# Optimization experiments

Hardware: AMD Instinct MI355X
Metric: run time of the kernel (lower is better)

Reference implementation:

```python
import jax, jax.numpy as jnp
import numpy as np

H, W, D, HEADS = 32, 32, 16, 8
EPS = 1e-5

def _ln(x, g, b):
    m = jnp.mean(x, -1, keepdims=True)
    v = jnp.mean((x - m) ** 2, -1, keepdims=True)
    return (x - m) / jnp.sqrt(v + EPS) * g + b

def _attn(x, w_qkv, w_proj, b_proj):
    # x: (Bb, N, C); torch Linear: y = x @ W.T + b
    Bb, N, C = x.shape
    hd = C // HEADS
    qkv = jnp.einsum('bnc,dc->bnd', x, w_qkv).reshape(Bb, N, 3, HEADS, hd)
    q, k, v = qkv[:, :, 0], qkv[:, :, 1], qkv[:, :, 2]  # (Bb,N,h,hd)
    att = jnp.einsum('bnhd,bmhd->bhnm', q, k) * (hd ** -0.5)
    att = jax.nn.softmax(att, axis=-1)
    o = jnp.einsum('bhnm,bmhd->bnhd', att, v).reshape(Bb, N, C)
    return jnp.einsum('bnc,dc->bnd', o, w_proj) + b_proj

def setup_inputs() -> dict:
    key = jax.random.key(0)
    ks = jax.random.split(key, 8)
    C, HID = 96, 384
    s = 0.02
    return {
        'x': jax.random.normal(ks[0], (1, C, D, H, W), jnp.float32),
        'norm1_g': jnp.ones((C,), jnp.float32),
        'norm1_b': jnp.zeros((C,), jnp.float32),
        'qkv_hw_w': jax.random.normal(ks[1], (3 * C, C), jnp.float32) * s,
        'proj_hw_w': jax.random.normal(ks[2], (C, C), jnp.float32) * s,
        'proj_hw_b': jnp.zeros((C,), jnp.float32),
        'qkv_t_w': jax.random.normal(ks[3], (3 * C, C), jnp.float32) * s,
        'proj_t_w': jax.random.normal(ks[4], (C, C), jnp.float32) * s,
        'proj_t_b': jnp.zeros((C,), jnp.float32),
        'norm2_g': jnp.ones((C,), jnp.float32),
        'norm2_b': jnp.zeros((C,), jnp.float32),
        'fc1_w': jax.random.normal(ks[5], (HID, C), jnp.float32) * s,
        'fc1_b': jnp.zeros((HID,), jnp.float32),
        'fc2_w': jax.random.normal(ks[6], (C, HID), jnp.float32) * s,
        'fc2_b': jnp.zeros((C,), jnp.float32),
    }

def reference(x, norm1_g, norm1_b, qkv_hw_w, proj_hw_w, proj_hw_b,
              qkv_t_w, proj_t_w, proj_t_b, norm2_g, norm2_b,
              fc1_w, fc1_b, fc2_w, fc2_b):
    B, C = x.shape[0], x.shape[1]
    HWn = H * W
    xf = x.reshape(B, C, -1).transpose(0, 2, 1)  # (B, L, C), L = D*H*W (D-major)
    shortcut = xf
    n1 = _ln(xf, norm1_g, norm1_b).reshape(B, D, HWn, C)
    # attention over H*W tokens (batched over B*D)
    a_hw = _attn(n1.reshape(B * D, HWn, C), qkv_hw_w, proj_hw_w, proj_hw_b)
    a_hw = a_hw.reshape(B, -1, C)  # D-major token order
    # attention over D tokens (batched over B*H*W)
    a_t = _attn(n1.transpose(0, 2, 1, 3).reshape(B * HWn, D, C), qkv_t_w, proj_t_w, proj_t_b)
    a_t = a_t.reshape(B, HWn * D, C)  # HW-major order (faithful to original view)
    out_res = shortcut + a_hw + a_t
    h1 = jax.nn.gelu(jnp.einsum('blc,hc->blh', _ln(out_res, norm2_g, norm2_b), fc1_w) + fc1_b,
                     approximate=False)
    mlp_out = jnp.einsum('blh,ch->blc', h1, fc2_w) + fc2_b
    out_ffn = out_res + mlp_out
    out = out_ffn.reshape(B, H, W, D, C).transpose(0, 4, 3, 1, 2)  # (B,C,D,H,W)
    return out
```

## Files before the change

### kernel.cpp

```cpp
#include <hip/hip_runtime.h>
#include <math.h>

#define L_TOK 16384
#define C_DIM 96
#define N_HEADS 8
#define HD 12
#define D_DIM 16
#define HW_N 1024
#define HID_DIM 384
#define SCALE 0.2886751345948129f
#define LOG2E 1.4426950408889634f

typedef _Float16 h4 __attribute__((ext_vector_type(4)));
typedef __fp16 fp16x2 __attribute__((ext_vector_type(2)));
typedef float v4f __attribute__((ext_vector_type(4)));

static __device__ __forceinline__ float fast_exp2(float x) {
#if __has_builtin(__builtin_amdgcn_exp2f)
    return __builtin_amdgcn_exp2f(x);
#else
    float r;
    asm("v_exp_f32 %0, %1" : "=v"(r) : "v"(x));
    return r;
#endif
}

static __device__ __forceinline__ h4 pack4(float a, float b, float c, float d) {
    fp16x2 lo = __builtin_amdgcn_cvt_pkrtz(a, b);
    fp16x2 hi = __builtin_amdgcn_cvt_pkrtz(c, d);
    union { fp16x2 p[2]; h4 v; } u;
    u.p[0] = lo; u.p[1] = hi;
    return u.v;
}

__global__ __launch_bounds__(256) void prep_kernel(
    const float* __restrict__ x, const float* __restrict__ g1,
    const float* __restrict__ b1, _Float16* __restrict__ n1h,
    const float* __restrict__ qkv_hw_w, const float* __restrict__ qkv_t_w,
    const float* __restrict__ proj_hw_w, const float* __restrict__ proj_t_w,
    const float* __restrict__ proj_hw_b, const float* __restrict__ proj_t_b,
    const float* __restrict__ fc1_w, const float* __restrict__ fc2_w,
    _Float16* __restrict__ wq, _Float16* __restrict__ wp,
    _Float16* __restrict__ wf1, _Float16* __restrict__ wf2,
    float* __restrict__ bp) {
    if (blockIdx.x < 64) {
        int l = blockIdx.x * 256 + threadIdx.x;
        float v[C_DIM];
        float s = 0.f;
#pragma unroll
        for (int c = 0; c < C_DIM; c++) {
            v[c] = x[(size_t)c * L_TOK + l];
            s += v[c];
        }
        float mean = s * (1.f / C_DIM);
        float var = 0.f;
#pragma unroll
        for (int c = 0; c < C_DIM; c++) {
            float dd = v[c] - mean;
            var += dd * dd;
        }
        float r = rsqrtf(var * (1.f / C_DIM) + 1e-5f);
        _Float16* op = n1h + (size_t)l * C_DIM;
#pragma unroll
        for (int c = 0; c < C_DIM; c += 4) {
            h4 o;
            o[0] = (_Float16)((v[c + 0] - mean) * r * g1[c + 0] + b1[c + 0]);
            o[1] = (_Float16)((v[c + 1] - mean) * r * g1[c + 1] + b1[c + 1]);
            o[2] = (_Float16)((v[c + 2] - mean) * r * g1[c + 2] + b1[c + 2]);
            o[3] = (_Float16)((v[c + 3] - mean) * r * g1[c + 3] + b1[c + 3]);
            *(h4*)(op + c) = o;
        }
        return;
    }
    int idx = (blockIdx.x - 64) * 256 + threadIdx.x;
    if (idx < 55296) {
        int n = idx / 96;
        float v = (n < 288) ? qkv_hw_w[idx] : qkv_t_w[idx - 27648];
        bool isq = (n < 96) || (n >= 288 && n < 384);
        wq[idx] = (_Float16)(isq ? v * (SCALE * LOG2E) : v);
    } else if (idx < 55296 + 18432) {
        int i = idx - 55296;
        int n = i / 192, k = i % 192;
        float v = (k < 96) ? proj_hw_w[n * 96 + k] : proj_t_w[n * 96 + k - 96];
        wp[i] = (_Float16)v;
    } else if (idx < 73728 + 36864) {
        int i = idx - 73728;
        wf1[i] = (_Float16)fc1_w[i];
    } else if (idx < 110592 + 36864) {
        int i = idx - 110592;
        wf2[i] = (_Float16)fc2_w[i];
    } else if (idx < 147456 + 96) {
        int i = idx - 147456;
        bp[i] = proj_hw_b[i] + proj_t_b[i];
    }
}

#define GBM 64
#define GBN 48
#define GBK 96
#define LSTRIDE 104

__global__ __launch_bounds__(256) void gemm_qkv(
    const _Float16* __restrict__ A, const _Float16* __restrict__ W,
    _Float16* __restrict__ Qp, _Float16* __restrict__ Kp,
    _Float16* __restrict__ VTp, _Float16* __restrict__ Tp) {
    __shared__ _Float16 As[GBM][LSTRIDE];
    __shared__ _Float16 Ws[GBN][LSTRIDE];
    const int t = threadIdx.x;
    const int m0 = blockIdx.x * GBM;
    const int n0 = blockIdx.y * GBN;
    const int lane = t & 63, w = t >> 6, g = lane >> 4, r = lane & 15;

    v4f acc[3];
#pragma unroll
    for (int nt = 0; nt < 3; nt++) {
        acc[nt][0] = 0.f; acc[nt][1] = 0.f; acc[nt][2] = 0.f; acc[nt][3] = 0.f;
    }
#pragma unroll
    for (int i = 0; i < 3; i++) {
        int idx = t + i * 256;
        int row = idx / 12, c = idx % 12;
        *(float4*)&As[row][c * 8] =
            *(const float4*)&A[(size_t)(m0 + row) * 96 + c * 8];
    }
#pragma unroll
    for (int i = 0; i < 3; i++) {
        int idx = t + i * 256;
        if (idx < 576) {
            int row = idx / 12, c = idx % 12;
            *(float4*)&Ws[row][c * 8] =
                *(const float4*)&W[(size_t)(n0 + row) * 96 + c * 8];
        }
    }
    __syncthreads();
#pragma unroll
    for (int ks = 0; ks < 6; ks++) {
        h4 af = *(const h4*)&As[w * 16 + r][ks * 16 + 4 * g];
#pragma unroll
        for (int nt = 0; nt < 3; nt++) {
            h4 wf = *(const h4*)&Ws[nt * 16 + r][ks * 16 + 4 * g];
            acc[nt] = __builtin_amdgcn_mfma_f32_16x16x16f16(wf, af, acc[nt], 0, 0, 0);
        }
    }

    const int m = m0 + w * 16 + r;
    const int d = m >> 10, hw = m & 1023;
    const int by = blockIdx.y;
#pragma unroll
    for (int nt = 0; nt < 3; nt++) {
        const int nb = n0 + nt * 16 + 4 * g;
        h4 ov;
        ov[0] = (_Float16)acc[nt][0]; ov[1] = (_Float16)acc[nt][1];
        ov[2] = (_Float16)acc[nt][2]; ov[3] = (_Float16)acc[nt][3];
        if (by < 2) {
            int n = nb;
            int h = (unsigned)n / 12u, dd = n - h * 12;
            *(h4*)&Qp[((size_t)(d * 8 + h) * 1024 + hw) * 12 + dd] = ov;
        } else if (by < 4) {
            int n = nb - 96;
            int h = (unsigned)n / 12u, dd = n - h * 12;
            *(h4*)&Kp[((size_t)(d * 8 + h) * 1024 + hw) * 12 + dd] = ov;
        } else if (by < 6) {
            int n = nb - 192;
            int h = (unsigned)n / 12u, dd = n - h * 12;
#pragma unroll
            for (int j = 0; j < 4; j++) {
                VTp[((size_t)(d * 8 + h) * 12 + dd + j) * 1024 + hw] = ov[j];
            }
        } else {
            *(h4*)&Tp[(size_t)(hw * 16 + d) * 288 + (nb - 288)] = ov;
        }
    }
}

#define WSTRIDE 104

#define STAGE(buf, src, stride)                                              \
    {                                                                        \
        _Pragma("unroll")                                                    \
        for (int i_ = 0; i_ < 5; i_++) {                                     \
            int idx_ = t + i_ * 256;                                         \
            if (idx_ < 1152) {                                               \
                int row_ = idx_ / 12, c_ = idx_ % 12;                        \
                *(float4*)&Wb[buf][row_ * WSTRIDE + c_ * 8] =                \
                    *(const float4*)&(src)[(size_t)row_ * (stride) + c_ * 8];\
            }                                                                \
        }                                                                    \
    }

#define PROJ_CHUNK(buf, kc)                                                  \
    {                                                                        \
        _Pragma("unroll")                                                    \
        for (int ks = 0; ks < 6; ks++) {                                     \
            _Pragma("unroll")                                                \
            for (int nt = 0; nt < 6; nt++) {                                 \
                h4 wf = *(const h4*)&Wb[buf][(nt * 16 + r) * WSTRIDE +       \
                                             ks * 16 + 4 * g];               \
                acc[nt] = __builtin_amdgcn_mfma_f32_16x16x16f16(             \
                    wf, afp[kc][ks], acc[nt], 0, 0, 0);                      \
            }                                                                \
        }                                                                    \
    }

#define FC1_CHUNK(buf, nc)                                                   \
    {                                                                        \
        v4f f[6];                                                            \
        _Pragma("unroll")                                                    \
        for (int nt = 0; nt < 6; nt++) {                                     \
            f[nt][0] = 0.f; f[nt][1] = 0.f; f[nt][2] = 0.f; f[nt][3] = 0.f;  \
        }                                                                    \
        _Pragma("unroll")                                                    \
        for (int ks = 0; ks < 6; ks++) {                                     \
            _Pragma("unroll")                                                \
            for (int nt = 0; nt < 6; nt++) {                                 \
                h4 wf = *(const h4*)&Wb[buf][(nt * 16 + r) * WSTRIDE +       \
                                             ks * 16 + 4 * g];               \
                f[nt] = __builtin_amdgcn_mfma_f32_16x16x16f16(               \
                    wf, n2f[ks], f[nt], 0, 0, 0);                            \
            }                                                                \
        }                                                                    \
        _Pragma("unroll")                                                    \
        for (int nt = 0; nt < 6; nt++) {                                     \
            const int nb = (nc) * 96 + nt * 16 + 4 * g;                      \
            float4 bv = *(const float4*)&f1b[nb];                            \
            float u0 = f[nt][0] + bv.x, u1 = f[nt][1] + bv.y;                \
            float u2 = f[nt][2] + bv.z, u3 = f[nt][3] + bv.w;                \
            hf[nc][nt] =                                                     \
                pack4(0.5f * u0 * (1.f + erff(u0 * 0.7071067811865476f)),    \
                      0.5f * u1 * (1.f + erff(u1 * 0.7071067811865476f)),    \
                      0.5f * u2 * (1.f + erff(u2 * 0.7071067811865476f)),    \
                      0.5f * u3 * (1.f + erff(u3 * 0.7071067811865476f)));   \
        }                                                                    \
    }

#define FC2_CHUNK(buf, kc)                                                   \
    {                                                                        \
        _Pragma("unroll")                                                    \
        for (int ks = 0; ks < 6; ks++) {                                     \
            _Pragma("unroll")                                                \
            for (int nt = 0; nt < 6; nt++) {                                 \
                h4 wf = *(const h4*)&Wb[buf][(nt * 16 + r) * WSTRIDE +       \
                                             ks * 16 + 4 * g];               \
                o6[nt] = __builtin_amdgcn_mfma_f32_16x16x16f16(              \
                    wf, hf[kc][ks], o6[nt], 0, 0, 0);                        \
            }                                                                \
        }                                                                    \
    }

__global__ __launch_bounds__(256) void fused_mlp(
    const _Float16* __restrict__ A, const _Float16* __restrict__ wp,
    const float* __restrict__ bp, const float* __restrict__ x,
    const float* __restrict__ g2, const float* __restrict__ b2,
    const _Float16* __restrict__ wf1, const float* __restrict__ f1b,
    const _Float16* __restrict__ wf2, const float* __restrict__ f2b,
    float* __restrict__ out) {
    __shared__ _Float16 Wb[2][96 * WSTRIDE];
    __shared__ float sh[96 * 68];

    const int t = threadIdx.x;
    const int bx = blockIdx.x;
    const int bxs = (bx & 7) * 32 + (bx >> 3);
    const int m0 = bxs * 64;
    const int lane = t & 63, w = t >> 6, g = lane >> 4, r = lane & 15;
    const int ml = w * 16 + r;
    const int m = m0 + ml;

    h4 afp[2][6];
#pragma unroll
    for (int kc = 0; kc < 2; kc++)
#pragma unroll
        for (int ks = 0; ks < 6; ks++)
            afp[kc][ks] =
                *(const h4*)&A[(size_t)m * 192 + kc * 96 + ks * 16 + 4 * g];
    float xr[24];
#pragma unroll
    for (int nt = 0; nt < 6; nt++) {
#pragma unroll
        for (int j = 0; j < 4; j++)
            xr[nt * 4 + j] = x[(size_t)(nt * 16 + 4 * g + j) * L_TOK + m];
    }

    STAGE(0, wp, 192);
    __syncthreads();
    STAGE(1, wp + 96, 192);
    v4f acc[6];
#pragma unroll
    for (int nt = 0; nt < 6; nt++) {
        acc[nt][0] = 0.f; acc[nt][1] = 0.f; acc[nt][2] = 0.f; acc[nt][3] = 0.f;
    }
    PROJ_CHUNK(0, 0);
    __syncthreads();
    STAGE(0, wf1, 96);
    PROJ_CHUNK(1, 1);
    float v[24];
    float sum = 0.f;
#pragma unroll
    for (int nt = 0; nt < 6; nt++) {
        const int nb = nt * 16 + 4 * g;
        float4 bv = *(const float4*)&bp[nb];
        float a0 = acc[nt][0] + bv.x + xr[nt * 4 + 0];
        float a1 = acc[nt][1] + bv.y + xr[nt * 4 + 1];
        float a2 = acc[nt][2] + bv.z + xr[nt * 4 + 2];
        float a3 = acc[nt][3] + bv.w + xr[nt * 4 + 3];
        v[nt * 4 + 0] = a0; v[nt * 4 + 1] = a1;
        v[nt * 4 + 2] = a2; v[nt * 4 + 3] = a3;
        sum += (a0 + a1) + (a2 + a3);
    }
    sum += __shfl_xor(sum, 16, 64);
    sum += __shfl_xor(sum, 32, 64);
    float mean = sum * (1.f / 96.f);
    float ss = 0.f;
#pragma unroll
    for (int i = 0; i < 24; i++) {
        float dd = v[i] - mean;
        ss += dd * dd;
    }
    ss += __shfl_xor(ss, 16, 64);
    ss += __shfl_xor(ss, 32, 64);
    float rstd = rsqrtf(ss * (1.f / 96.f) + 1e-5f);
    h4 n2f[6];
#pragma unroll
    for (int nt = 0; nt < 6; nt++) {
        const int nb = nt * 16 + 4 * g;
        float4 gg = *(const float4*)&g2[nb];
        float4 bb = *(const float4*)&b2[nb];
        n2f[nt] = pack4((v[nt * 4 + 0] - mean) * rstd * gg.x + bb.x,
                        (v[nt * 4 + 1] - mean) * rstd * gg.y + bb.y,
                        (v[nt * 4 + 2] - mean) * rstd * gg.z + bb.z,
                        (v[nt * 4 + 3] - mean) * rstd * gg.w + bb.w);
    }
    __syncthreads();
    h4 hf[4][6];
    STAGE(1, wf1 + 96 * 96, 96);
    FC1_CHUNK(0, 0);
    __syncthreads();
    STAGE(0, wf1 + 2 * 96 * 96, 96);
    FC1_CHUNK(1, 1);
    __syncthreads();
    STAGE(1, wf1 + 3 * 96 * 96, 96);
    FC1_CHUNK(0, 2);
    __syncthreads();
    STAGE(0, wf2, 384);
    FC1_CHUNK(1, 3);
    __syncthreads();
    v4f o6[6];
#pragma unroll
    for (int nt = 0; nt < 6; nt++) {
        o6[nt][0] = 0.f; o6[nt][1] = 0.f; o6[nt][2] = 0.f; o6[nt][3] = 0.f;
    }
    STAGE(1, wf2 + 96, 384);
    FC2_CHUNK(0, 0);
    __syncthreads();
    STAGE(0, wf2 + 192, 384);
    FC2_CHUNK(1, 1);
    __syncthreads();
    STAGE(1, wf2 + 288, 384);
    FC2_CHUNK(0, 2);
    __syncthreads();
    FC2_CHUNK(1, 3);

#pragma unroll
    for (int nt = 0; nt < 6; nt++) {
        const int nb = nt * 16 + 4 * g;
        float4 bv = *(const float4*)&f2b[nb];
        sh[(nb + 0) * 68 + ml] = o6[nt][0] + bv.x + v[nt * 4 + 0];
        sh[(nb + 1) * 68 + ml] = o6[nt][1] + bv.y + v[nt * 4 + 1];
        sh[(nb + 2) * 68 + ml] = o6[nt][2] + bv.z + v[nt * 4 + 2];
        sh[(nb + 3) * 68 + ml] = o6[nt][3] + bv.w + v[nt * 4 + 3];
    }
    __syncthreads();
    const int hh = m0 >> 9, ww0 = (m0 >> 4) & 31;
#pragma unroll
    for (int i = 0; i < 6; i++) {
        int task = t + i * 256;
        int n = task >> 4, dd = task & 15;
        float4 ov;
        ov.x = sh[n * 68 + dd];
        ov.y = sh[n * 68 + dd + 16];
        ov.z = sh[n * 68 + dd + 32];
        ov.w = sh[n * 68 + dd + 48];
        *(float4*)&out[(size_t)n * L_TOK + dd * 1024 + hh * 32 + ww0] = ov;
    }
}

__global__ __launch_bounds__(256) void attn_hw_kernel(
    const _Float16* __restrict__ Qp, const _Float16* __restrict__ Kp,
    const _Float16* __restrict__ VTp, _Float16* __restrict__ o_cat) {
    __shared__ _Float16 K_lds[1024 * 12];
    __shared__ _Float16 VT_lds[13 * 1032];
    const int t = threadIdx.x;
    const int qb = blockIdx.x, h = blockIdx.y, d = blockIdx.z;
    const size_t tokbase = (size_t)d * HW_N;
    const int hoff = h * HD;
    const size_t slice = (size_t)(d * 8 + h);

    {
        const float4* Kg = (const float4*)(Kp + slice * 12288);
        float4* K4 = (float4*)K_lds;
#pragma unroll
        for (int i = 0; i < 6; i++) K4[t + i * 256] = Kg[t + i * 256];
        const float4* Vg = (const float4*)(VTp + slice * 12288);
#pragma unroll
        for (int i = 0; i < 6; i++) {
            int off = t + i * 256;
            int row = off >> 7, col = (off & 127) * 8;
            *(float4*)&VT_lds[row * 1032 + col] = Vg[off];
        }
        unsigned* zp = (unsigned*)&VT_lds[12 * 1032];
        zp[t] = 0x3C003C00u; zp[t + 256] = 0x3C003C00u;
        if (t < 4) zp[t + 512] = 0x3C003C00u;
    }

    const int lane = t & 63, w = t >> 6, g = lane >> 4, r = lane & 15;
    const int q0w = qb * 128 + w * 32;

    h4 zf; zf[0] = zf[1] = zf[2] = zf[3] = (_Float16)0.f;
    h4 qf[2];
    {
        const _Float16* Qbase = Qp + (slice * 1024 + q0w + r) * 12 + 4 * g;
#pragma unroll
        for (int qt = 0; qt < 2; qt++) {
            qf[qt] = (g < 3) ? *(const h4*)(Qbase + qt * 16 * 12) : zf;
        }
    }

    v4f acc[2];
#pragma unroll
    for (int qt = 0; qt < 2; qt++) {
        acc[qt][0] = acc[qt][1] = acc[qt][2] = acc[qt][3] = 0.f;
    }

    const int koff = r * 12 + 4 * g;
    const int rowc = (r < 12) ? r : 12;
    const int voff = rowc * 1032 + 4 * g;

    __syncthreads();

    v4f zero; zero[0] = zero[1] = zero[2] = zero[3] = 0.f;
#pragma unroll 4
    for (int kt = 0; kt < HW_N / 16; kt++) {
        h4 kf = (g < 3) ? *(const h4*)&K_lds[kt * 192 + koff] : zf;
        h4 vf = *(const h4*)&VT_lds[voff + kt * 16];
#pragma unroll
        for (int qt = 0; qt < 2; qt++) {
            v4f s = __builtin_amdgcn_mfma_f32_16x16x16f16(kf, qf[qt], zero, 0, 0, 0);
            h4 pf = pack4(fast_exp2(s[0]), fast_exp2(s[1]),
                          fast_exp2(s[2]), fast_exp2(s[3]));
            acc[qt] = __builtin_amdgcn_mfma_f32_16x16x16f16(vf, pf, acc[qt], 0, 0, 0);
        }
    }

#pragma unroll
    for (int qt = 0; qt < 2; qt++) {
        float denom = __shfl(acc[qt][0], 48 + r, 64);
        float rs = 1.f / denom;
        if (g < 3) {
            _Float16* op =
                o_cat + (tokbase + q0w + qt * 16 + r) * 192 + hoff + 4 * g;
            h4 o;
            o[0] = (_Float16)(acc[qt][0] * rs);
            o[1] = (_Float16)(acc[qt][1] * rs);
            o[2] = (_Float16)(acc[qt][2] * rs);
            o[3] = (_Float16)(acc[qt][3] * rs);
            *(h4*)op = o;
        }
    }
}

__global__ __launch_bounds__(256) void attn_t_kernel(
    const _Float16* __restrict__ Tp, _Float16* __restrict__ o_cat) {
    int gid = blockIdx.x * 256 + threadIdx.x;
    int hw = gid >> 7;
    int h = (gid >> 4) & 7;
    int q = gid & 15;
    const int hoff = h * HD;
    const _Float16* base = Tp + (size_t)(hw * 16) * 288;

    float qr[HD];
    {
        const _Float16* p = base + q * 288 + hoff;
        h4 a = *(const h4*)p, b = *(const h4*)(p + 4), c = *(const h4*)(p + 8);
#pragma unroll
        for (int e = 0; e < 4; e++) {
            qr[e] = (float)a[e]; qr[4 + e] = (float)b[e]; qr[8 + e] = (float)c[e];
        }
    }
    float s[D_DIM];
    float mx = -1e30f;
#pragma unroll
    for (int j = 0; j < D_DIM; j++) {
        const _Float16* kp = base + j * 288 + 96 + hoff;
        h4 a = *(const h4*)kp, b = *(const h4*)(kp + 4), c = *(const h4*)(kp + 8);
        float dot = 0.f;
#pragma unroll
        for (int e = 0; e < 4; e++) {
            dot += qr[e] * (float)a[e] + qr[4 + e] * (float)b[e] +
                   qr[8 + e] * (float)c[e];
        }
        s[j] = dot;
        mx = fmaxf(mx, dot);
    }
    float sum = 0.f;
#pragma unroll
    for (int j = 0; j < D_DIM; j++) {
        s[j] = fast_exp2(s[j] - mx);
        sum += s[j];
    }
    float rs = 1.f / sum;
    float o[HD];
#pragma unroll
    for (int e = 0; e < HD; e++) o[e] = 0.f;
#pragma unroll
    for (int j = 0; j < D_DIM; j++) {
        const _Float16* vp = base + j * 288 + 192 + hoff;
        h4 a = *(const h4*)vp, b = *(const h4*)(vp + 4), c = *(const h4*)(vp + 8);
        float p = s[j];
#pragma unroll
        for (int e = 0; e < 4; e++) {
            o[e] += p * (float)a[e];
            o[4 + e] += p * (float)b[e];
            o[8 + e] += p * (float)c[e];
        }
    }
    _Float16* op = o_cat + ((size_t)hw * D_DIM + q) * 192 + 96 + hoff;
#pragma unroll
    for (int e = 0; e < HD; e += 4) {
        h4 a;
        a[0] = (_Float16)(o[e] * rs); a[1] = (_Float16)(o[e + 1] * rs);
        a[2] = (_Float16)(o[e + 2] * rs); a[3] = (_Float16)(o[e + 3] * rs);
        *(h4*)(op + e) = a;
    }
}

extern "C" void kernel_launch(void* const* d_in, const int* in_sizes, int n_in,
                              void* d_out, int out_size, void* d_ws,
                              size_t ws_size, hipStream_t stream) {
    const float* x         = (const float*)d_in[0];
    const float* norm1_g   = (const float*)d_in[1];
    const float* norm1_b   = (const float*)d_in[2];
    const float* qkv_hw_w  = (const float*)d_in[3];
    const float* proj_hw_w = (const float*)d_in[4];
    const float* proj_hw_b = (const float*)d_in[5];
    const float* qkv_t_w   = (const float*)d_in[6];
    const float* proj_t_w  = (const float*)d_in[7];
    const float* proj_t_b  = (const float*)d_in[8];
    const float* norm2_g   = (const float*)d_in[9];
    const float* norm2_b   = (const float*)d_in[10];
    const float* fc1_w     = (const float*)d_in[11];
    const float* fc1_b     = (const float*)d_in[12];
    const float* fc2_w     = (const float*)d_in[13];
    const float* fc2_b     = (const float*)d_in[14];
    float* out = (float*)d_out;

    char* ws = (char*)d_ws;
    _Float16* n1h    = (_Float16*)ws;
    _Float16* o_cat  = n1h + (size_t)L_TOK * C_DIM;
    float*    out_res= (float*)(o_cat + (size_t)L_TOK * 192);
    _Float16* packs  = (_Float16*)(out_res + (size_t)L_TOK * C_DIM);
    _Float16* Qp     = packs;
    _Float16* Kp     = Qp + 1572864;
    _Float16* VTp    = Kp + 1572864;
    _Float16* Tp     = VTp + 1572864;
    _Float16* wq     = Tp + (size_t)L_TOK * 288;
    _Float16* wp     = wq + 55296;
    _Float16* wf1    = wp + 18432;
    _Float16* wf2    = wf1 + 36864;
    float*    bp     = (float*)(wf2 + 36864);

    prep_kernel<<<641, 256, 0, stream>>>(x, norm1_g, norm1_b, n1h,
                                         qkv_hw_w, qkv_t_w, proj_hw_w,
                                         proj_t_w, proj_hw_b, proj_t_b,
                                         fc1_w, fc2_w, wq, wp, wf1, wf2, bp);
    gemm_qkv<<<dim3(L_TOK / GBM, 576 / GBN), 256, 0, stream>>>(
        n1h, wq, Qp, Kp, VTp, Tp);
    attn_hw_kernel<<<dim3(8, N_HEADS, D_DIM), 256, 0, stream>>>(
        Qp, Kp, VTp, o_cat);
    attn_t_kernel<<<(HW_N * N_HEADS * D_DIM) / 256, 256, 0, stream>>>(Tp, o_cat);
    fused_mlp<<<L_TOK / 64, 256, 0, stream>>>(
        o_cat, wp, bp, x, norm2_g, norm2_b, wf1, fc1_b, wf2, fc2_b, out);
}
```

Before: 92.83 us.

## Halve fused MLP tile to 32 tokens and alias output staging onto weight LDS

```diff
diff --git a/kernel.cpp b/kernel.cpp
--- a/kernel.cpp
+++ b/kernel.cpp
@@ -174,28 +174,29 @@
 }
 
 #define WSTRIDE 104
+#define SH_STRIDE 42
 
 #define STAGE(buf, src, stride)                                              \
     {                                                                        \
+        _Float16* Wb_ = (buf) ? Wb1 : Wb0;                                   \
         _Pragma("unroll")                                                    \
-        for (int i_ = 0; i_ < 5; i_++) {                                     \
-            int idx_ = t + i_ * 256;                                         \
-            if (idx_ < 1152) {                                               \
-                int row_ = idx_ / 12, c_ = idx_ % 12;                        \
-                *(float4*)&Wb[buf][row_ * WSTRIDE + c_ * 8] =                \
-                    *(const float4*)&(src)[(size_t)row_ * (stride) + c_ * 8];\
-            }                                                                \
+        for (int i_ = 0; i_ < 9; i_++) {                                     \
+            int idx_ = t + i_ * 128;                                         \
+            int row_ = idx_ / 12, c_ = idx_ % 12;                            \
+            *(float4*)&Wb_[row_ * WSTRIDE + c_ * 8] =                        \
+                *(const float4*)&(src)[(size_t)row_ * (stride) + c_ * 8];    \
         }                                                                    \
     }
 
 #define PROJ_CHUNK(buf, kc)                                                  \
     {                                                                        \
+        const _Float16* Wb_ = (buf) ? Wb1 : Wb0;                             \
         _Pragma("unroll")                                                    \
         for (int ks = 0; ks < 6; ks++) {                                     \
             _Pragma("unroll")                                                \
             for (int nt = 0; nt < 6; nt++) {                                 \
-                h4 wf = *(const h4*)&Wb[buf][(nt * 16 + r) * WSTRIDE +       \
-                                             ks * 16 + 4 * g];               \
+                h4 wf = *(const h4*)&Wb_[(nt * 16 + r) * WSTRIDE +           \
+                                         ks * 16 + 4 * g];                   \
                 acc[nt] = __builtin_amdgcn_mfma_f32_16x16x16f16(             \
                     wf, afp[kc][ks], acc[nt], 0, 0, 0);                      \
             }                                                                \
@@ -204,6 +205,7 @@
 
 #define FC1_CHUNK(buf, nc)                                                   \
     {                                                                        \
+        const _Float16* Wb_ = (buf) ? Wb1 : Wb0;                             \
         v4f f[6];                                                            \
         _Pragma("unroll")                                                    \
         for (int nt = 0; nt < 6; nt++) {                                     \
@@ -213,8 +215,8 @@
         for (int ks = 0; ks < 6; ks++) {                                     \
             _Pragma("unroll")                                                \
             for (int nt = 0; nt < 6; nt++) {                                 \
-                h4 wf = *(const h4*)&Wb[buf][(nt * 16 + r) * WSTRIDE +       \
-                                             ks * 16 + 4 * g];               \
+                h4 wf = *(const h4*)&Wb_[(nt * 16 + r) * WSTRIDE +           \
+                                         ks * 16 + 4 * g];                   \
                 f[nt] = __builtin_amdgcn_mfma_f32_16x16x16f16(               \
                     wf, n2f[ks], f[nt], 0, 0, 0);                            \
             }                                                                \
@@ -235,32 +237,35 @@
 
 #define FC2_CHUNK(buf, kc)                                                   \
     {                                                                        \
+        const _Float16* Wb_ = (buf) ? Wb1 : Wb0;                             \
         _Pragma("unroll")                                                    \
         for (int ks = 0; ks < 6; ks++) {                                     \
             _Pragma("unroll")                                                \
             for (int nt = 0; nt < 6; nt++) {                                 \
-                h4 wf = *(const h4*)&Wb[buf][(nt * 16 + r) * WSTRIDE +       \
-                                             ks * 16 + 4 * g];               \
+                h4 wf = *(const h4*)&Wb_[(nt * 16 + r) * WSTRIDE +           \
+                                         ks * 16 + 4 * g];                   \
                 o6[nt] = __builtin_amdgcn_mfma_f32_16x16x16f16(              \
                     wf, hf[kc][ks], o6[nt], 0, 0, 0);                        \
             }                                                                \
         }                                                                    \
     }
 
-__global__ __launch_bounds__(256) void fused_mlp(
+__global__ __launch_bounds__(128, 2) void fused_mlp(
     const _Float16* __restrict__ A, const _Float16* __restrict__ wp,
     const float* __restrict__ bp, const float* __restrict__ x,
     const float* __restrict__ g2, const float* __restrict__ b2,
     const _Float16* __restrict__ wf1, const float* __restrict__ f1b,
     const _Float16* __restrict__ wf2, const float* __restrict__ f2b,
     float* __restrict__ out) {
-    __shared__ _Float16 Wb[2][96 * WSTRIDE];
-    __shared__ float sh[96 * 68];
+    __shared__ __align__(16) char pool[39936];
+    _Float16* Wb0 = (_Float16*)pool;
+    _Float16* Wb1 = (_Float16*)(pool + 19968);
+    float* sh = (float*)pool;
 
     const int t = threadIdx.x;
     const int bx = blockIdx.x;
-    const int bxs = (bx & 7) * 32 + (bx >> 3);
-    const int m0 = bxs * 64;
+    const int bxs = (bx & 7) * 64 + (bx >> 3);
+    const int m0 = bxs * 32;
     const int lane = t & 63, w = t >> 6, g = lane >> 4, r = lane & 15;
     const int ml = w * 16 + r;
     const int m = m0 + ml;
@@ -363,23 +368,21 @@
     for (int nt = 0; nt < 6; nt++) {
         const int nb = nt * 16 + 4 * g;
         float4 bv = *(const float4*)&f2b[nb];
-        sh[(nb + 0) * 68 + ml] = o6[nt][0] + bv.x + v[nt * 4 + 0];
-        sh[(nb + 1) * 68 + ml] = o6[nt][1] + bv.y + v[nt * 4 + 1];
-        sh[(nb + 2) * 68 + ml] = o6[nt][2] + bv.z + v[nt * 4 + 2];
-        sh[(nb + 3) * 68 + ml] = o6[nt][3] + bv.w + v[nt * 4 + 3];
+        sh[(nb + 0) * SH_STRIDE + ml] = o6[nt][0] + bv.x + v[nt * 4 + 0];
+        sh[(nb + 1) * SH_STRIDE + ml] = o6[nt][1] + bv.y + v[nt * 4 + 1];
+        sh[(nb + 2) * SH_STRIDE + ml] = o6[nt][2] + bv.z + v[nt * 4 + 2];
+        sh[(nb + 3) * SH_STRIDE + ml] = o6[nt][3] + bv.w + v[nt * 4 + 3];
     }
     __syncthreads();
     const int hh = m0 >> 9, ww0 = (m0 >> 4) & 31;
 #pragma unroll
-    for (int i = 0; i < 6; i++) {
-        int task = t + i * 256;
+    for (int i = 0; i < 12; i++) {
+        int task = t + i * 128;
         int n = task >> 4, dd = task & 15;
-        float4 ov;
-        ov.x = sh[n * 68 + dd];
-        ov.y = sh[n * 68 + dd + 16];
-        ov.z = sh[n * 68 + dd + 32];
-        ov.w = sh[n * 68 + dd + 48];
-        *(float4*)&out[(size_t)n * L_TOK + dd * 1024 + hh * 32 + ww0] = ov;
+        float2 ov;
+        ov.x = sh[n * SH_STRIDE + dd];
+        ov.y = sh[n * SH_STRIDE + 16 + dd];
+        *(float2*)&out[(size_t)n * L_TOK + dd * 1024 + hh * 32 + ww0] = ov;
     }
 }
 
@@ -576,6 +579,6 @@
     attn_hw_kernel<<<dim3(8, N_HEADS, D_DIM), 256, 0, stream>>>(
         Qp, Kp, VTp, o_cat);
     attn_t_kernel<<<(HW_N * N_HEADS * D_DIM) / 256, 256, 0, stream>>>(Tp, o_cat);
-    fused_mlp<<<L_TOK / 64, 256, 0, stream>>>(
+    fused_mlp<<<512, 128, 0, stream>>>(
         o_cat, wp, bp, x, norm2_g, norm2_b, wf1, fc1_b, wf2, fc2_b, out);
 }
```

Measured after the change: 104.4 us. 1.12x slower.
